# Performance work log

Hardware: AMD Instinct MI355X
Metric: run time of the kernel (lower is better)

Reference implementation:

```python
import math
import jax, jax.numpy as jnp
import numpy as np

B, T, C = 8, 1024, 512
H = 8
NUM_FRAMES = 128  # num_tokens
NUM_ANIMALS = 8   # num_id; NUM_FRAMES * NUM_ANIMALS == T


def _linear_params(key, fan_in, fan_out):
    kw, kb = jax.random.split(key)
    bound = 1.0 / math.sqrt(fan_in)
    W = jax.random.uniform(kw, (fan_out, fan_in), jnp.float32, -bound, bound)
    b = jax.random.uniform(kb, (fan_out,), jnp.float32, -bound, bound)
    return W, b


def setup_inputs() -> dict:
    key = jax.random.key(0)
    ks = jax.random.split(key, 6)
    x = jax.random.normal(ks[0], (B, T, C), jnp.float32)
    mask = jnp.ones((B, T), jnp.float32)
    Wq, bq = _linear_params(ks[1], C, C)
    Wk, bk = _linear_params(ks[2], C, C)
    Wv, bv = _linear_params(ks[3], C, C)
    Wp, bp = _linear_params(ks[4], C, C)
    return {"x": x, "mask": mask, "Wq": Wq, "bq": bq, "Wk": Wk, "bk": bk,
            "Wv": Wv, "bv": bv, "Wp": Wp, "bp": bp}


def _block_causal_mask():
    # tril over frames, expanded so all animals within a frame attend to all
    # animals of frames <= current frame: kron(tril(F,F), ones(I,I)) -> (T,T)
    tril = jnp.tril(jnp.ones((NUM_FRAMES, NUM_FRAMES), jnp.float32))
    return jnp.kron(tril, jnp.ones((NUM_ANIMALS, NUM_ANIMALS), jnp.float32))


def reference(x, mask, Wq, bq, Wk, bk, Wv, bv, Wp, bp):
    Bx, Tx, Cx = x.shape
    d = Cx // H
    q = (x @ Wq.T + bq).reshape(Bx, Tx, H, d).transpose(0, 2, 1, 3)  # b h t d
    k = (x @ Wk.T + bk).reshape(Bx, Tx, H, d).transpose(0, 2, 1, 3)
    v = (x @ Wv.T + bv).reshape(Bx, Tx, H, d).transpose(0, 2, 1, 3)
    att = jnp.einsum('bhqd,bhkd->bhqk', q, k) * (1.0 / math.sqrt(d))
    m = _block_causal_mask()[None, None] * mask[:, None, None, :]  # (B,1,T,T)
    att = jnp.where(m == 0, -jnp.inf, att)
    att = jax.nn.softmax(att, axis=-1)
    # dropout is identity (pdrop=0.0 / eval mode)
    y = jnp.einsum('bhqk,bhkd->bhqd', att, v)
    y = y.transpose(0, 2, 1, 3).reshape(Bx, Tx, Cx)
    return y @ Wp.T + bp
```

## Files before the change

kernel.cpp:

```cpp
#include <hip/hip_runtime.h>
#include <cstdint>
#include <cstddef>

#define BB 8
#define TT 1024
#define CC 512
#define HH 8
#define DD 64
#define MM (BB*TT)

typedef short s16x4 __attribute__((ext_vector_type(4)));
typedef _Float16 f16x8 __attribute__((ext_vector_type(8)));
typedef float f32x4  __attribute__((ext_vector_type(4)));

__device__ __forceinline__ short f2hs(float f) {
  _Float16 h = (_Float16)f;
  return __builtin_bit_cast(short, h);
}

__device__ __forceinline__ f32x4 mfma16h(f16x8 a, f16x8 b, f32x4 c) {
  return __builtin_amdgcn_mfma_f32_16x16x32_f16(a, b, c, 0, 0, 0);
}

__device__ __forceinline__ void gload_lds16(const void* g, void* l) {
  __builtin_amdgcn_global_load_lds(
      (const __attribute__((address_space(1))) unsigned int*)g,
      (__attribute__((address_space(3))) unsigned int*)l, 16, 0, 0);
}

__global__ void prep_kernel(const float* __restrict__ x,
                            const float* __restrict__ mask,
                            const float* __restrict__ Wq,
                            const float* __restrict__ Wk,
                            const float* __restrict__ Wv,
                            const float* __restrict__ Wp,
                            short* __restrict__ Xh,
                            short* __restrict__ Wqkv,
                            short* __restrict__ Wpc,
                            float* __restrict__ maskAdd) {
  const int NXv = MM * CC / 4;
  const int NWv = CC * CC / 4;
  const int NM = BB * TT;
  int stride = gridDim.x * blockDim.x;
  for (int i = blockIdx.x * blockDim.x + threadIdx.x; i < NXv + 4 * NWv + NM; i += stride) {
    if (i < NXv) {
      int e = i * 4;
      float4 v = *(const float4*)(x + e);
      s16x4 h = {f2hs(v.x), f2hs(v.y), f2hs(v.z), f2hs(v.w)};
      *(s16x4*)(Xh + e) = h;
    } else if (i < NXv + 4 * NWv) {
      int wi = i - NXv;
      int wsel = wi >> 16;
      int idx = wi & 65535;
      int r = idx >> 7, c = (idx & 127) << 2;
      const float* W = (wsel == 0) ? Wq : (wsel == 1) ? Wk : (wsel == 2) ? Wv : Wp;
      float4 v = *(const float4*)(W + (size_t)r * CC + c);
      s16x4 h = {f2hs(v.x), f2hs(v.y), f2hs(v.z), f2hs(v.w)};
      short* dst = (wsel < 3) ? (Wqkv + (size_t)(wsel * 512 + r) * CC + c)
                              : (Wpc + (size_t)r * CC + c);
      *(s16x4*)dst = h;
    } else {
      int mi = i - NXv - 4 * NWv;
      maskAdd[mi] = (mask[mi] == 0.f) ? -1e30f : 0.f;
    }
  }
}

template <int BN, int EPI>
__global__ __launch_bounds__(512, 4) void gemm_kernel(
    const short* __restrict__ A, const short* __restrict__ Bw,
    const float* __restrict__ b0, const float* __restrict__ b1,
    const float* __restrict__ b2,
    short* __restrict__ qo, short* __restrict__ ko, short* __restrict__ vt,
    float* __restrict__ outp) {
  constexpr int MR = 4;
  constexpr int NR = BN / 64;
  constexpr int ABYT = 128 * 128;
  constexpr int TILE = ABYT + BN * 128;
  constexpr int NT = 8;
  constexpr int BL = BN / 64;
  __shared__ __align__(1024) char smem[2 * TILE];

  const int tid = threadIdx.x;
  const int lane = tid & 63;
  const int w = tid >> 6;
  const int wm = w >> 2, wn = w & 3;
  const int l15 = lane & 15, lg = lane >> 4;
  const int lsw = (l15 & 7) << 4;
  const int sr8 = lane >> 3;
  const int scbsw = ((lane & 7) * 16) ^ (sr8 << 4);

  const int rowA = blockIdx.x * 128;
  const int rowB = blockIdx.y * BN;
  const char* Ab = (const char*)A + (size_t)(rowA + sr8) * 1024 + scbsw;
  const char* Bb = (const char*)Bw + (size_t)(rowB + sr8) * 1024 + scbsw;

  f32x4 acc[MR][NR] = {};

  auto STAGE_A = [&](char* dst, int kt) {
#pragma unroll
    for (int g = 0; g < 2; ++g) {
      int r0 = (w * 2 + g) * 8;
      gload_lds16(Ab + (size_t)r0 * 1024 + (size_t)kt * 128, dst + r0 * 128);
    }
  };
  auto STAGE_B = [&](char* dst, int kt) {
#pragma unroll
    for (int g = 0; g < BL; ++g) {
      int r0 = (w * BL + g) * 8;
      gload_lds16(Bb + (size_t)r0 * 1024 + (size_t)kt * 128, dst + ABYT + r0 * 128);
    }
  };
  auto RDA2 = [&](const char* buf, int mh, int kk, f16x8* af) {
#pragma unroll
    for (int i = 0; i < 2; ++i) {
      int row = wm * 64 + (mh * 2 + i) * 16 + l15;
      af[i] = *(const f16x8*)(buf + row * 128 + ((kk * 64 + lg * 16) ^ lsw));
    }
  };
  auto RDBk = [&](const char* buf, int kk, f16x8* bfr) {
#pragma unroll
    for (int j = 0; j < NR; ++j) {
      int row = wn * (BN / 4) + j * 16 + l15;
      bfr[j] = *(const f16x8*)(buf + ABYT + row * 128 + ((kk * 64 + lg * 16) ^ lsw));
    }
  };

  STAGE_A(smem, 0);
  STAGE_B(smem, 0);
  asm volatile("s_waitcnt vmcnt(0)" ::: "memory");
  __builtin_amdgcn_s_barrier();

  for (int t = 0; t < NT; ++t) {
    char* bufp = smem + (t & 1) * TILE;
    char* bufn = smem + ((t + 1) & 1) * TILE;
    f16x8 af[2], bfr[NR];

#define PH(MH)                                                                \
  __builtin_amdgcn_s_barrier();                                               \
  asm volatile("s_waitcnt lgkmcnt(0)" ::: "memory");                          \
  __builtin_amdgcn_sched_barrier(0);                                          \
  __builtin_amdgcn_s_setprio(1);                                              \
  _Pragma("unroll")                                                           \
  for (int i = 0; i < 2; ++i)                                                 \
    _Pragma("unroll")                                                         \
    for (int j = 0; j < NR; ++j)                                              \
      acc[(MH) * 2 + i][j] = mfma16h(af[i], bfr[j], acc[(MH) * 2 + i][j]);    \
  __builtin_amdgcn_s_setprio(0);

    RDBk(bufp, 0, bfr);
    RDA2(bufp, 0, 0, af);
    if (t + 1 < NT) STAGE_A(bufn, t + 1);
    PH(0)
    RDA2(bufp, 1, 0, af);
    if (t + 1 < NT) STAGE_B(bufn, t + 1);
    PH(1)
    RDBk(bufp, 1, bfr);
    RDA2(bufp, 1, 1, af);
    PH(1)
    RDA2(bufp, 0, 1, af);
    PH(0)
#undef PH
    asm volatile("s_waitcnt vmcnt(0)" ::: "memory");
    __builtin_amdgcn_s_barrier();
  }

#pragma unroll
  for (int m = 0; m < MR; ++m) {
    int rbase = rowA + wm * 64 + m * 16 + lg * 4;
#pragma unroll
    for (int n = 0; n < NR; ++n) {
      int col = rowB + wn * (BN / 4) + n * 16 + l15;
#pragma unroll
      for (int j = 0; j < 4; ++j) {
        float v = acc[m][n][j];
        int r = rbase + j;
        if constexpr (EPI == 0) {
          int b = r >> 10, t = r & 1023;
          int wsel = col >> 9, c = col & 511;
          int h = c >> 6, dd = c & 63;
          int bh = b * HH + h;
          if (wsel == 0) {
            qo[((size_t)bh * TT + t) * DD + dd] = f2hs(v + b0[c]);
          } else if (wsel == 1) {
            ko[((size_t)bh * TT + t) * DD + dd] = f2hs(v + b1[c]);
          } else {
            vt[((size_t)bh * DD + dd) * TT + t] = f2hs(v + b2[c]);
          }
        } else {
          outp[(size_t)r * CC + col] = v + b0[col];
        }
      }
    }
  }
}

__global__ __launch_bounds__(256, 2) void attn_kernel(
    const short* __restrict__ q, const short* __restrict__ k,
    const short* __restrict__ vt, const float* __restrict__ maskAdd,
    short* __restrict__ Yh) {
  const int blk = blockIdx.x;
  const int qb = blk & 15;
  const int bh = blk >> 4;
  const int b = bh >> 3, h = bh & 7;
  const int tid = threadIdx.x;
  const int lane = tid & 63;
  const int w = tid >> 6;
  const int l15 = lane & 15, lg = lane >> 4;
  const int lsw = (l15 & 7) << 4;

  __shared__ short Ks[2][64 * 64];
  __shared__ short Vs[2][64 * 64];
  __shared__ short Pl[4][16 * 64];

  const short* kbh = k + (size_t)bh * TT * DD;
  const short* vbh = vt + (size_t)bh * DD * TT;

  const int sr = lane >> 3;
  const int scb = (lane & 7) * 16;
  const int ssw = sr << 4;

  const int qrow = qb * 64 + w * 16 + l15;
  const short* qptr = q + ((size_t)bh * TT + qrow) * DD;
  f16x8 qf[2];
  qf[0] = *(const f16x8*)(qptr + lg * 8);
  qf[1] = *(const f16x8*)(qptr + 32 + lg * 8);

  f32x4 yacc[4] = {};
  float mrun = -1e30f, lrun = 0.f;

#pragma unroll
  for (int ph = 0; ph < 2; ++ph) {
    int row = w * 8 + ph * 32 + sr;
    gload_lds16((const char*)kbh + (size_t)row * 128 + (scb ^ ssw),
                (char*)&Ks[0][0] + (w * 8 + ph * 32) * 128);
    gload_lds16((const char*)vbh + (size_t)row * 2048 + (scb ^ ssw),
                (char*)&Vs[0][0] + (w * 8 + ph * 32) * 128);
  }
  __syncthreads();

  int buf = 0;
  for (int jt = 0; jt <= qb; ++jt) {
    if (jt < qb) {
      int nt = jt + 1;
#pragma unroll
      for (int ph = 0; ph < 2; ++ph) {
        int row = w * 8 + ph * 32 + sr;
        gload_lds16((const char*)kbh + (size_t)(nt * 64 + row) * 128 + (scb ^ ssw),
                    (char*)&Ks[buf ^ 1][0] + (w * 8 + ph * 32) * 128);
        gload_lds16((const char*)vbh + (size_t)row * 2048 + nt * 128 + (scb ^ ssw),
                    (char*)&Vs[buf ^ 1][0] + (w * 8 + ph * 32) * 128);
      }
    }
    f32x4 mav[4];
#pragma unroll
    for (int n = 0; n < 4; ++n)
      mav[n] = *(const f32x4*)(maskAdd + (size_t)b * TT + jt * 64 + n * 16 + lg * 4);

    f32x4 sacc[4] = {};
#pragma unroll
    for (int c = 0; c < 2; ++c) {
      f16x8 qc = qf[c];
#pragma unroll
      for (int n = 0; n < 4; ++n) {
        int krow = n * 16 + l15;
        const f16x8 kf = *(const f16x8*)((const char*)&Ks[buf][0] + krow * 128 + ((c * 64 + lg * 16) ^ lsw));
        sacc[n] = mfma16h(kf, qc, sacc[n]);
      }
    }
    const int qloc8 = (w * 16 + l15) >> 3;
#pragma unroll
    for (int n = 0; n < 4; ++n)
#pragma unroll
      for (int jj = 0; jj < 4; ++jj) {
        float s = sacc[n][jj] * 0.125f + mav[n][jj];
        if (jt == qb) {
          int kloc = n * 16 + lg * 4 + jj;
          if ((kloc >> 3) > qloc8) s = -1e30f;
        }
        sacc[n][jj] = s;
      }
    float pm = sacc[0][0];
#pragma unroll
    for (int n = 0; n < 4; ++n)
#pragma unroll
      for (int jj = 0; jj < 4; ++jj) pm = fmaxf(pm, sacc[n][jj]);
    pm = fmaxf(pm, __shfl_xor(pm, 16));
    pm = fmaxf(pm, __shfl_xor(pm, 32));
    float mnew = fmaxf(mrun, pm);
    float alpha = __expf(mrun - mnew);
    mrun = mnew;
    float psum = 0.f;
#pragma unroll
    for (int n = 0; n < 4; ++n) {
      float p0 = __expf(sacc[n][0] - mrun);
      float p1 = __expf(sacc[n][1] - mrun);
      float p2 = __expf(sacc[n][2] - mrun);
      float p3 = __expf(sacc[n][3] - mrun);
      psum += (p0 + p1) + (p2 + p3);
      uint2 pw;
      pw.x = (unsigned)(unsigned short)f2hs(p0) | ((unsigned)(unsigned short)f2hs(p1) << 16);
      pw.y = (unsigned)(unsigned short)f2hs(p2) | ((unsigned)(unsigned short)f2hs(p3) << 16);
      *(uint2*)((char*)&Pl[w][0] + l15 * 128 + ((n * 32 + lg * 8) ^ lsw)) = pw;
    }
    psum += __shfl_xor(psum, 16);
    psum += __shfl_xor(psum, 32);
    lrun = lrun * alpha + psum;
    float ab[4];
#pragma unroll
    for (int jj = 0; jj < 4; ++jj) ab[jj] = __shfl(alpha, lg * 4 + jj);
#pragma unroll
    for (int dt = 0; dt < 4; ++dt)
#pragma unroll
      for (int jj = 0; jj < 4; ++jj) yacc[dt][jj] *= ab[jj];
#pragma unroll
    for (int c = 0; c < 2; ++c) {
      const f16x8 pa = *(const f16x8*)((const char*)&Pl[w][0] + l15 * 128 + ((c * 64 + lg * 16) ^ lsw));
#pragma unroll
      for (int dt = 0; dt < 4; ++dt) {
        int vrow = dt * 16 + l15;
        const f16x8 vf = *(const f16x8*)((const char*)&Vs[buf][0] + vrow * 128 + ((c * 64 + lg * 16) ^ lsw));
        yacc[dt] = mfma16h(pa, vf, yacc[dt]);
      }
    }
    __syncthreads();
    buf ^= 1;
  }

  float lb[4];
#pragma unroll
  for (int jj = 0; jj < 4; ++jj) lb[jj] = 1.f / __shfl(lrun, lg * 4 + jj);
#pragma unroll
  for (int dt = 0; dt < 4; ++dt) {
    int col = h * DD + dt * 16 + l15;
#pragma unroll
    for (int jj = 0; jj < 4; ++jj) {
      int row = b * TT + qb * 64 + w * 16 + lg * 4 + jj;
      float y = yacc[dt][jj] * lb[jj];
      Yh[(size_t)row * CC + col] = f2hs(y);
    }
  }
}

extern "C" void kernel_launch(void* const* d_in, const int* in_sizes, int n_in,
                              void* d_out, int out_size, void* d_ws, size_t ws_size,
                              hipStream_t stream) {
  const float* x    = (const float*)d_in[0];
  const float* mask = (const float*)d_in[1];
  const float* Wq   = (const float*)d_in[2];
  const float* bq   = (const float*)d_in[3];
  const float* Wk   = (const float*)d_in[4];
  const float* bk   = (const float*)d_in[5];
  const float* Wv   = (const float*)d_in[6];
  const float* bv   = (const float*)d_in[7];
  const float* Wp   = (const float*)d_in[8];
  const float* bp   = (const float*)d_in[9];
  float* out = (float*)d_out;

  char* ws = (char*)d_ws;
  short* Xh   = (short*)(ws);
  short* Wqkv = (short*)(ws + (size_t)8 * 1048576);
  short* Wpc  = (short*)(ws + (size_t)10 * 1048576);
  short* qo   = (short*)(ws + (size_t)11 * 1048576);
  short* ko   = (short*)(ws + (size_t)19 * 1048576);
  short* vt   = (short*)(ws + (size_t)27 * 1048576);
  short* Yh   = (short*)(ws + (size_t)35 * 1048576);
  float* maskAdd = (float*)(ws + (size_t)43 * 1048576);

  prep_kernel<<<2048, 256, 0, stream>>>(x, mask, Wq, Wk, Wv, Wp, Xh, Wqkv, Wpc, maskAdd);

  gemm_kernel<192, 0><<<dim3(64, 8), 512, 0, stream>>>(
      Xh, Wqkv, bq, bk, bv, qo, ko, vt, nullptr);

  attn_kernel<<<dim3(64 * 16), 256, 0, stream>>>(qo, ko, vt, maskAdd, Yh);

  gemm_kernel<128, 1><<<dim3(64, 4), 512, 0, stream>>>(
      Yh, Wpc, bp, nullptr, nullptr, nullptr, nullptr, nullptr, out);
}
```

Baseline: 88.91 us.

## Pair complementary causal query tiles per block to balance attention work

Each attention block now has 8 waves and handles two query tiles, qb=8+p and qb=7-p, so every block walks the same total number of KV tiles and the triangular causal workload is balanced. The two tiles share the K/V tiles staged in shared memory, which cuts redundant global loads for the lower tile. Waves whose tile has finished sit idle through the remaining iterations but still hit the barriers. s_setprio is also raised around the MFMA sections to favour matrix issue.

```diff
diff --git a/kernel.cpp b/kernel.cpp
--- a/kernel.cpp
+++ b/kernel.cpp
@@ -195,133 +195,133 @@
   }
 }
 
-__global__ __launch_bounds__(256, 2) void attn_kernel(
+__global__ __launch_bounds__(512, 2) void attn_kernel(
     const short* __restrict__ q, const short* __restrict__ k,
     const short* __restrict__ vt, const float* __restrict__ maskAdd,
     short* __restrict__ Yh) {
   const int blk = blockIdx.x;
-  const int qb = blk & 15;
-  const int bh = blk >> 4;
+  const int p = blk & 7;
+  const int bh = blk >> 3;
   const int b = bh >> 3, h = bh & 7;
+  const int qbA = 8 + p;
+  const int qbB = 7 - p;
   const int tid = threadIdx.x;
   const int lane = tid & 63;
   const int w = tid >> 6;
+  const int wloc = w & 3;
+  const int qtile = (w < 4) ? qbA : qbB;
   const int l15 = lane & 15, lg = lane >> 4;
   const int lsw = (l15 & 7) << 4;
 
   __shared__ short Ks[2][64 * 64];
   __shared__ short Vs[2][64 * 64];
-  __shared__ short Pl[4][16 * 64];
+  __shared__ short Pl[8][16 * 64];
 
   const short* kbh = k + (size_t)bh * TT * DD;
   const short* vbh = vt + (size_t)bh * DD * TT;
 
-  const int sr = lane >> 3;
-  const int scb = (lane & 7) * 16;
-  const int ssw = sr << 4;
-
-  const int qrow = qb * 64 + w * 16 + l15;
+  const int srow = tid >> 3;
+  const int scb = ((tid & 7) * 16) ^ ((srow & 7) << 4);
+
+  const int qrow = qtile * 64 + wloc * 16 + l15;
   const short* qptr = q + ((size_t)bh * TT + qrow) * DD;
-  f16x8 qf[2];
-  qf[0] = *(const f16x8*)(qptr + lg * 8);
-  qf[1] = *(const f16x8*)(qptr + 32 + lg * 8);
+  f16x8 qf0 = *(const f16x8*)(qptr + lg * 8);
+  f16x8 qf1 = *(const f16x8*)(qptr + 32 + lg * 8);
 
   f32x4 yacc[4] = {};
   float mrun = -1e30f, lrun = 0.f;
 
-#pragma unroll
-  for (int ph = 0; ph < 2; ++ph) {
-    int row = w * 8 + ph * 32 + sr;
-    gload_lds16((const char*)kbh + (size_t)row * 128 + (scb ^ ssw),
-                (char*)&Ks[0][0] + (w * 8 + ph * 32) * 128);
-    gload_lds16((const char*)vbh + (size_t)row * 2048 + (scb ^ ssw),
-                (char*)&Vs[0][0] + (w * 8 + ph * 32) * 128);
-  }
+  gload_lds16((const char*)kbh + (size_t)srow * 128 + scb,
+              (char*)&Ks[0][0] + srow * 128);
+  gload_lds16((const char*)vbh + (size_t)srow * 2048 + scb,
+              (char*)&Vs[0][0] + srow * 128);
   __syncthreads();
 
   int buf = 0;
-  for (int jt = 0; jt <= qb; ++jt) {
-    if (jt < qb) {
+  for (int jt = 0; jt <= qbA; ++jt) {
+    if (jt < qbA) {
       int nt = jt + 1;
-#pragma unroll
-      for (int ph = 0; ph < 2; ++ph) {
-        int row = w * 8 + ph * 32 + sr;
-        gload_lds16((const char*)kbh + (size_t)(nt * 64 + row) * 128 + (scb ^ ssw),
-                    (char*)&Ks[buf ^ 1][0] + (w * 8 + ph * 32) * 128);
-        gload_lds16((const char*)vbh + (size_t)row * 2048 + nt * 128 + (scb ^ ssw),
-                    (char*)&Vs[buf ^ 1][0] + (w * 8 + ph * 32) * 128);
+      gload_lds16((const char*)kbh + (size_t)(nt * 64 + srow) * 128 + scb,
+                  (char*)&Ks[buf ^ 1][0] + srow * 128);
+      gload_lds16((const char*)vbh + (size_t)srow * 2048 + nt * 128 + scb,
+                  (char*)&Vs[buf ^ 1][0] + srow * 128);
+    }
+    if (jt <= qtile) {
+      f32x4 mav[4];
+#pragma unroll
+      for (int n = 0; n < 4; ++n)
+        mav[n] = *(const f32x4*)(maskAdd + (size_t)b * TT + jt * 64 + n * 16 + lg * 4);
+
+      f32x4 sacc[4] = {};
+      __builtin_amdgcn_s_setprio(1);
+#pragma unroll
+      for (int c = 0; c < 2; ++c) {
+        f16x8 qc = (c == 0) ? qf0 : qf1;
+#pragma unroll
+        for (int n = 0; n < 4; ++n) {
+          int krow = n * 16 + l15;
+          const f16x8 kf = *(const f16x8*)((const char*)&Ks[buf][0] + krow * 128 + ((c * 64 + lg * 16) ^ lsw));
+          sacc[n] = mfma16h(kf, qc, sacc[n]);
+        }
       }
-    }
-    f32x4 mav[4];
-#pragma unroll
-    for (int n = 0; n < 4; ++n)
-      mav[n] = *(const f32x4*)(maskAdd + (size_t)b * TT + jt * 64 + n * 16 + lg * 4);
-
-    f32x4 sacc[4] = {};
-#pragma unroll
-    for (int c = 0; c < 2; ++c) {
-      f16x8 qc = qf[c];
+      __builtin_amdgcn_s_setprio(0);
+      const int qloc8 = (wloc * 16 + l15) >> 3;
+#pragma unroll
+      for (int n = 0; n < 4; ++n)
+#pragma unroll
+        for (int jj = 0; jj < 4; ++jj) {
+          float s = sacc[n][jj] * 0.125f + mav[n][jj];
+          if (jt == qtile) {
+            int kloc = n * 16 + lg * 4 + jj;
+            if ((kloc >> 3) > qloc8) s = -1e30f;
+          }
+          sacc[n][jj] = s;
+        }
+      float pm = sacc[0][0];
+#pragma unroll
+      for (int n = 0; n < 4; ++n)
+#pragma unroll
+        for (int jj = 0; jj < 4; ++jj) pm = fmaxf(pm, sacc[n][jj]);
+      pm = fmaxf(pm, __shfl_xor(pm, 16));
+      pm = fmaxf(pm, __shfl_xor(pm, 32));
+      float mnew = fmaxf(mrun, pm);
+      float alpha = __expf(mrun - mnew);
+      mrun = mnew;
+      float psum = 0.f;
 #pragma unroll
       for (int n = 0; n < 4; ++n) {
-        int krow = n * 16 + l15;
-        const f16x8 kf = *(const f16x8*)((const char*)&Ks[buf][0] + krow * 128 + ((c * 64 + lg * 16) ^ lsw));
-        sacc[n] = mfma16h(kf, qc, sacc[n]);
+        float p0 = __expf(sacc[n][0] - mrun);
+        float p1 = __expf(sacc[n][1] - mrun);
+        float p2 = __expf(sacc[n][2] - mrun);
+        float p3 = __expf(sacc[n][3] - mrun);
+        psum += (p0 + p1) + (p2 + p3);
+        uint2 pw;
+        pw.x = (unsigned)(unsigned short)f2hs(p0) | ((unsigned)(unsigned short)f2hs(p1) << 16);
+        pw.y = (unsigned)(unsigned short)f2hs(p2) | ((unsigned)(unsigned short)f2hs(p3) << 16);
+        *(uint2*)((char*)&Pl[w][0] + l15 * 128 + ((n * 32 + lg * 8) ^ lsw)) = pw;
       }
-    }
-    const int qloc8 = (w * 16 + l15) >> 3;
-#pragma unroll
-    for (int n = 0; n < 4; ++n)
-#pragma unroll
-      for (int jj = 0; jj < 4; ++jj) {
-        float s = sacc[n][jj] * 0.125f + mav[n][jj];
-        if (jt == qb) {
-          int kloc = n * 16 + lg * 4 + jj;
-          if ((kloc >> 3) > qloc8) s = -1e30f;
+      psum += __shfl_xor(psum, 16);
+      psum += __shfl_xor(psum, 32);
+      lrun = lrun * alpha + psum;
+      float ab[4];
+#pragma unroll
+      for (int jj = 0; jj < 4; ++jj) ab[jj] = __shfl(alpha, lg * 4 + jj);
+#pragma unroll
+      for (int dt = 0; dt < 4; ++dt)
+#pragma unroll
+        for (int jj = 0; jj < 4; ++jj) yacc[dt][jj] *= ab[jj];
+      __builtin_amdgcn_s_setprio(1);
+#pragma unroll
+      for (int c = 0; c < 2; ++c) {
+        const f16x8 pa = *(const f16x8*)((const char*)&Pl[w][0] + l15 * 128 + ((c * 64 + lg * 16) ^ lsw));
+#pragma unroll
+        for (int dt = 0; dt < 4; ++dt) {
+          int vrow = dt * 16 + l15;
+          const f16x8 vf = *(const f16x8*)((const char*)&Vs[buf][0] + vrow * 128 + ((c * 64 + lg * 16) ^ lsw));
+          yacc[dt] = mfma16h(pa, vf, yacc[dt]);
         }
-        sacc[n][jj] = s;
       }
-    float pm = sacc[0][0];
-#pragma unroll
-    for (int n = 0; n < 4; ++n)
-#pragma unroll
-      for (int jj = 0; jj < 4; ++jj) pm = fmaxf(pm, sacc[n][jj]);
-    pm = fmaxf(pm, __shfl_xor(pm, 16));
-    pm = fmaxf(pm, __shfl_xor(pm, 32));
-    float mnew = fmaxf(mrun, pm);
-    float alpha = __expf(mrun - mnew);
-    mrun = mnew;
-    float psum = 0.f;
-#pragma unroll
-    for (int n = 0; n < 4; ++n) {
-      float p0 = __expf(sacc[n][0] - mrun);
-      float p1 = __expf(sacc[n][1] - mrun);
-      float p2 = __expf(sacc[n][2] - mrun);
-      float p3 = __expf(sacc[n][3] - mrun);
-      psum += (p0 + p1) + (p2 + p3);
-      uint2 pw;
-      pw.x = (unsigned)(unsigned short)f2hs(p0) | ((unsigned)(unsigned short)f2hs(p1) << 16);
-      pw.y = (unsigned)(unsigned short)f2hs(p2) | ((unsigned)(unsigned short)f2hs(p3) << 16);
-      *(uint2*)((char*)&Pl[w][0] + l15 * 128 + ((n * 32 + lg * 8) ^ lsw)) = pw;
-    }
-    psum += __shfl_xor(psum, 16);
-    psum += __shfl_xor(psum, 32);
-    lrun = lrun * alpha + psum;
-    float ab[4];
-#pragma unroll
-    for (int jj = 0; jj < 4; ++jj) ab[jj] = __shfl(alpha, lg * 4 + jj);
-#pragma unroll
-    for (int dt = 0; dt < 4; ++dt)
-#pragma unroll
-      for (int jj = 0; jj < 4; ++jj) yacc[dt][jj] *= ab[jj];
-#pragma unroll
-    for (int c = 0; c < 2; ++c) {
-      const f16x8 pa = *(const f16x8*)((const char*)&Pl[w][0] + l15 * 128 + ((c * 64 + lg * 16) ^ lsw));
-#pragma unroll
-      for (int dt = 0; dt < 4; ++dt) {
-        int vrow = dt * 16 + l15;
-        const f16x8 vf = *(const f16x8*)((const char*)&Vs[buf][0] + vrow * 128 + ((c * 64 + lg * 16) ^ lsw));
-        yacc[dt] = mfma16h(pa, vf, yacc[dt]);
-      }
+      __builtin_amdgcn_s_setprio(0);
     }
     __syncthreads();
     buf ^= 1;
@@ -335,7 +335,7 @@
     int col = h * DD + dt * 16 + l15;
 #pragma unroll
     for (int jj = 0; jj < 4; ++jj) {
-      int row = b * TT + qb * 64 + w * 16 + lg * 4 + jj;
+      int row = b * TT + qtile * 64 + wloc * 16 + lg * 4 + jj;
       float y = yacc[dt][jj] * lb[jj];
       Yh[(size_t)row * CC + col] = f2hs(y);
     }
@@ -372,7 +372,7 @@
   gemm_kernel<192, 0><<<dim3(64, 8), 512, 0, stream>>>(
       Xh, Wqkv, bq, bk, bv, qo, ko, vt, nullptr);
 
-  attn_kernel<<<dim3(64 * 16), 256, 0, stream>>>(qo, ko, vt, maskAdd, Yh);
+  attn_kernel<<<dim3(512), 512, 0, stream>>>(qo, ko, vt, maskAdd, Yh);
 
   gemm_kernel<128, 1><<<dim3(64, 4), 512, 0, stream>>>(
       Yh, Wpc, bp, nullptr, nullptr, nullptr, nullptr, nullptr, out);
```

Measured after the change: 81.04 us. 8.9% less time.
